# Kernel tuning notes

Measured on AMD Instinct MI355X. Metric: run time of the kernel, lower is better.

Reference implementation:

```python
import math
import jax, jax.numpy as jnp
import numpy as np

B, S, E = 4, 2048, 768
H, D = 12, 64
LOCAL_H, GLOBAL_H = 8, 4
WINDOW_BASE, MIN_W, MAX_W = 128, 32, 512
GLOBAL_RATIO = 0.1
MASK_VALUE = -1e9


def setup_inputs() -> dict:
    key = jax.random.key(0)
    k1, k2, k3 = jax.random.split(key, 3)
    return {
        "x": jax.random.normal(k1, (B, S, E), dtype=jnp.float32),
        "w_attn": jax.random.normal(k2, (E, 3 * E), dtype=jnp.float32) * 0.02,
        "b_attn": jnp.zeros((3 * E,), dtype=jnp.float32),
        "w_proj": jax.random.normal(k3, (E, E), dtype=jnp.float32) * 0.02,
        "b_proj": jnp.zeros((E,), dtype=jnp.float32),
    }


def _masks(seq_len: int):
    # dynamic window (adaptive): base * sqrt(S/base), clamped
    w = int(WINDOW_BASE * math.sqrt(seq_len / WINDOW_BASE))
    w = max(MIN_W, min(w, MAX_W))
    half = w // 2
    i = jnp.arange(seq_len)[:, None]
    j = jnp.arange(seq_len)[None, :]
    # local: window band then causal override -> allowed iff i-half <= j <= i
    local_allowed = (j >= i - half) & (j <= i)
    local_mask = jnp.where(local_allowed, 0.0, MASK_VALUE).astype(jnp.float32)
    # global: columns at linspace positions allowed for all rows, plus full causal
    n_glob = max(1, int(seq_len * GLOBAL_RATIO))
    gpos = jnp.linspace(0.0, seq_len - 1, n_glob).astype(jnp.int32)
    is_gcol = jnp.zeros((seq_len,), dtype=bool).at[gpos].set(True)
    global_allowed = (j <= i) | is_gcol[None, :]
    global_mask = jnp.where(global_allowed, 0.0, MASK_VALUE).astype(jnp.float32)
    return local_mask, global_mask


def _attend(q, k, v, mask):
    # q,k,v: [B,h,S,D]; mask: [S,S]
    scale = 1.0 / math.sqrt(q.shape[-1])
    scores = jnp.einsum("bhqd,bhkd->bhqk", q, k) * scale + mask[None, None]
    w = jax.nn.softmax(scores, axis=-1)
    return jnp.einsum("bhqk,bhkd->bhqd", w, v)


def reference(x, w_attn, b_attn, w_proj, b_proj):
    b, s, _ = x.shape
    qkv = x @ w_attn + b_attn                       # [B,S,3E]
    q, k, v = jnp.split(qkv, 3, axis=-1)
    def heads(t):
        return t.reshape(b, s, H, D).transpose(0, 2, 1, 3)  # [B,H,S,D]
    q, k, v = heads(q), heads(k), heads(v)
    local_mask, global_mask = _masks(s)
    local_out = _attend(q[:, :LOCAL_H], k[:, :LOCAL_H], v[:, :LOCAL_H], local_mask)
    global_out = _attend(q[:, LOCAL_H:], k[:, LOCAL_H:], v[:, LOCAL_H:], global_mask)
    attn = jnp.concatenate([local_out, global_out], axis=1)  # heads 0..7 local, 8..11 global
    attn = attn.transpose(0, 2, 1, 3).reshape(b, s, E)
    return attn @ w_proj + b_proj
```

## Files before the change

### kernel.cpp

```cpp
#include <hip/hip_runtime.h>
#include <stdint.h>


#define NH 12
#define SQ 2048

typedef __bf16 bf16x8 __attribute__((ext_vector_type(8)));
typedef float f32x4 __attribute__((ext_vector_type(4)));

#define GLOAD_LDS16(g, l)                                                      \
  __builtin_amdgcn_global_load_lds(                                            \
      (__attribute__((address_space(1))) void*)(g),                            \
      (__attribute__((address_space(3))) void*)(l), 16, 0, 0)

__device__ __forceinline__ unsigned short bfbits(float f) {
  __bf16 h = (__bf16)f;
  return *(unsigned short*)&h;
}

__global__ void convert_x(const float* __restrict__ in, unsigned short* __restrict__ outp, int n4) {
  for (int i = blockIdx.x * blockDim.x + threadIdx.x; i < n4; i += gridDim.x * blockDim.x) {
    float4 v = ((const float4*)in)[i];
    ushort4 o = make_ushort4(bfbits(v.x), bfbits(v.y), bfbits(v.z), bfbits(v.w));
    ((ushort4*)outp)[i] = o;
  }
}

__global__ void convert_transpose(const float* __restrict__ in, unsigned short* __restrict__ out,
                                  int K, int N) {
  __shared__ float tile[32][33];
  int n0 = blockIdx.x * 32, k0 = blockIdx.y * 32;
  int tx = threadIdx.x, ty = threadIdx.y;
  for (int r = ty; r < 32; r += 8) tile[r][tx] = in[(size_t)(k0 + r) * N + n0 + tx];
  __syncthreads();
  for (int r = ty; r < 32; r += 8) out[(size_t)(n0 + r) * K + k0 + tx] = bfbits(tile[tx][r]);
}

__global__ __launch_bounds__(256) void vtrans(const unsigned short* __restrict__ QKV,
                                              unsigned short* __restrict__ Vtb) {
  const int bh = blockIdx.x;
  const int b = bh / NH, h = bh % NH;
  const int s0 = blockIdx.y * 64;
  __shared__ unsigned short T[64][72];
  const int t = threadIdx.x, r = t >> 2, c0 = (t & 3) * 16;
  const size_t src = (size_t)(b * SQ + s0 + r) * 2304 + 1536 + h * 64 + c0;
  *(uint4*)&T[r][c0]     = *(const uint4*)&QKV[src];
  *(uint4*)&T[r][c0 + 8] = *(const uint4*)&QKV[src + 8];
  __syncthreads();
  unsigned short pk[16];
#pragma unroll
  for (int z = 0; z < 16; ++z) pk[z] = T[c0 + z][r];
  size_t dst = (size_t)bh * 131072 + (size_t)r * 2048 + s0 + c0;
  *(uint4*)&Vtb[dst]     = *(uint4*)&pk[0];
  *(uint4*)&Vtb[dst + 8] = *(uint4*)&pk[8];
}

__global__ void gather_gcols(const unsigned short* __restrict__ QKV,
                             const unsigned short* __restrict__ Vtb,
                             unsigned short* __restrict__ Kg,
                             unsigned short* __restrict__ VgT,
                             int* __restrict__ gidx) {
  const int bh = blockIdx.x;
  const int b = bh >> 2, h = 8 + (bh & 3);
  const int tid = threadIdx.x;
  if (bh == 0 && blockIdx.y == 0) {
    int c = tid;
    gidx[c] = (c < 203) ? (int)((double)c * (2047.0 / 203.0)) : ((c == 203) ? 2047 : -1);
  }
  {
    int c = tid, ch = blockIdx.y;
    int col = (c < 203) ? (int)((double)c * (2047.0 / 203.0)) : ((c == 203) ? 2047 : -1);
    uint4 v = {0u, 0u, 0u, 0u};
    if (col >= 0) v = *(const uint4*)&QKV[(size_t)(b * SQ + col) * 2304 + 768 + h * 64 + ch * 8];
    *(uint4*)&Kg[((size_t)bh * 256 + c) * 64 + ch * 8] = v;
  }
  {
    const size_t base = (size_t)(b * NH + h) * 131072;
    int d = tid >> 2;
    int cb = (tid & 3) * 64 + blockIdx.y * 8;
    for (int cc = 0; cc < 8; ++cc) {
      int c = cb + cc;
      int col = (c < 203) ? (int)((double)c * (2047.0 / 203.0)) : ((c == 203) ? 2047 : -1);
      unsigned short v = 0;
      if (col >= 0) v = Vtb[base + (size_t)d * 2048 + col];
      VgT[((size_t)bh * 64 + d) * 256 + c] = v;
    }
  }
}

__device__ __forceinline__ void gemm_mainloop(
    const unsigned short* __restrict__ A, const unsigned short* __restrict__ BT,
    int m0, int n0, int tid,
    unsigned short* As, unsigned short* Bs,
    f32x4 acc[4][4]) {
  const int lane = tid & 63, wave = tid >> 6;
  const int wm = wave >> 1, wn = wave & 1;
  const int ln = lane & 15, quad = lane >> 4;
  const int arow = wave * 16 + (lane >> 2);
  const int acol = (lane & 3) * 8;

#pragma unroll
  for (int mi = 0; mi < 4; ++mi)
#pragma unroll
    for (int ni = 0; ni < 4; ++ni) acc[mi][ni] = (f32x4){0.f, 0.f, 0.f, 0.f};

  for (int kt = 0; kt < 24; ++kt) {
    const int k0 = kt * 32;
    __syncthreads();
#pragma unroll
    for (int p = 0; p < 2; ++p) {
      GLOAD_LDS16(A  + (size_t)(m0 + p * 64 + arow) * 768 + k0 + acol,
                  &As[(p * 64 + wave * 16) * 32]);
      GLOAD_LDS16(BT + (size_t)(n0 + p * 64 + arow) * 768 + k0 + acol,
                  &Bs[(p * 64 + wave * 16) * 32]);
    }
    __syncthreads();
    bf16x8 aF[4], bF[4];
#pragma unroll
    for (int mi = 0; mi < 4; ++mi) aF[mi] = *(const bf16x8*)&As[(wm * 64 + mi * 16 + ln) * 32 + quad * 8];
#pragma unroll
    for (int ni = 0; ni < 4; ++ni) bF[ni] = *(const bf16x8*)&Bs[(wn * 64 + ni * 16 + ln) * 32 + quad * 8];
#pragma unroll
    for (int mi = 0; mi < 4; ++mi)
#pragma unroll
      for (int ni = 0; ni < 4; ++ni)
        acc[mi][ni] = __builtin_amdgcn_mfma_f32_16x16x32_bf16(aF[mi], bF[ni], acc[mi][ni], 0, 0, 0);
  }
}

__global__ __launch_bounds__(256) void qkv_gemm(
    const unsigned short* __restrict__ Xb, const unsigned short* __restrict__ WT,
    const float* __restrict__ bias, unsigned short* __restrict__ Out) {
  __shared__ __attribute__((aligned(16))) unsigned short As[128 * 32];
  __shared__ __attribute__((aligned(16))) unsigned short Bs[128 * 32];
  f32x4 acc[4][4];
  const int m0 = blockIdx.y * 128, n0 = blockIdx.x * 128;
  const int tid = threadIdx.x;
  gemm_mainloop(Xb, WT, m0, n0, tid, As, Bs, acc);
  const int lane = tid & 63, wave = tid >> 6;
  const int wm = wave >> 1, wn = wave & 1, ln = lane & 15, quad = lane >> 4;
#pragma unroll
  for (int mi = 0; mi < 4; ++mi)
#pragma unroll
    for (int ni = 0; ni < 4; ++ni) {
      int n = n0 + wn * 64 + ni * 16 + ln;
      float bs = bias[n];
#pragma unroll
      for (int rg = 0; rg < 4; ++rg) {
        int m = m0 + wm * 64 + mi * 16 + quad * 4 + rg;
        Out[(size_t)m * 2304 + n] = bfbits(acc[mi][ni][rg] + bs);
      }
    }
}

__global__ __launch_bounds__(256) void proj_gemm(
    const unsigned short* __restrict__ Ab, const unsigned short* __restrict__ WT,
    const float* __restrict__ bias, float* __restrict__ Out) {
  __shared__ __attribute__((aligned(16))) unsigned short As[128 * 32];
  __shared__ __attribute__((aligned(16))) unsigned short Bs[128 * 32];
  f32x4 acc[4][4];
  const int m0 = blockIdx.y * 128, n0 = blockIdx.x * 128;
  const int tid = threadIdx.x;
  gemm_mainloop(Ab, WT, m0, n0, tid, As, Bs, acc);
  const int lane = tid & 63, wave = tid >> 6;
  const int wm = wave >> 1, wn = wave & 1, ln = lane & 15, quad = lane >> 4;
#pragma unroll
  for (int mi = 0; mi < 4; ++mi)
#pragma unroll
    for (int ni = 0; ni < 4; ++ni)
#pragma unroll
      for (int rg = 0; rg < 4; ++rg) {
        int m = m0 + wm * 64 + mi * 16 + quad * 4 + rg;
        int n = n0 + wn * 64 + ni * 16 + ln;
        Out[(size_t)m * 768 + n] = acc[mi][ni][rg] + bias[n];
      }
}

__global__ __launch_bounds__(256, 6) void attn_kernel(
    const unsigned short* __restrict__ QKV,
    const unsigned short* __restrict__ Vtb,
    const unsigned short* __restrict__ Kg, const unsigned short* __restrict__ VgT,
    const int* __restrict__ gidx,
    unsigned short* __restrict__ AOut,
    unsigned short* __restrict__ Opart,
    float* __restrict__ Lpart) {
  __shared__ __attribute__((aligned(16))) unsigned short Ks[64 * 72];
  __shared__ __attribute__((aligned(16))) unsigned short Vs[64 * 72];

  const int gid = blockIdx.x;
  int b, h, qb, kb_begin, kb_end, slot = -1;
  bool do_g;
  if (gid < 1184) {
    int bh = gid / 74, rem = gid % 74;
    b = bh >> 2; h = 8 + (bh & 3);
    int part;
    if (rem < 9)       { qb = rem; part = 0; }
    else if (rem < 27) { int z = rem - 9;  qb = 9 + (z >> 1);  part = z & 1; }
    else if (rem < 54) { int z = rem - 27; int q3 = z / 3; qb = 18 + q3; part = z - 3 * q3; }
    else               { int z = rem - 54; qb = 27 + (z >> 2); part = z & 3; }
    kb_begin = part * 9;
    kb_end = min(part * 9 + 8, qb);
    do_g = (part == 0);
    slot = (bh * 32 + qb) * 4 + part;
  } else {
    int lid = gid - 1184;
    int bh = lid >> 5; b = bh >> 3; h = bh & 7; qb = lid & 31;
    kb_begin = (qb > 4) ? qb - 4 : 0; kb_end = qb; do_g = false;
  }
  const int qb0 = qb * 64;
  const bool is_local = (h < 8);
  const int tid = threadIdx.x, lane = tid & 63, wave = tid >> 6;
  const int ln = lane & 15, quad = lane >> 4;
  const int bh48 = b * NH + h;
  const int bhg = (b << 2) | (h & 3);

  const size_t qoff = (size_t)(b * SQ + qb0 + wave * 16 + ln) * 2304 + h * 64;
  bf16x8 qA0 = *(const bf16x8*)&QKV[qoff + quad * 8];
  bf16x8 qA1 = *(const bf16x8*)&QKV[qoff + 32 + quad * 8];

  bf16x8 onesF;
#pragma unroll
  for (int z = 0; z < 8; ++z) onesF[z] = (__bf16)1.0f;

  f32x4 o[4];
  f32x4 ls = (f32x4){0.f, 0.f, 0.f, 0.f};
#pragma unroll
  for (int dt = 0; dt < 4; ++dt) o[dt] = (f32x4){0.f, 0.f, 0.f, 0.f};

  const int nc = kb_end - kb_begin + 1;
  const int ntiles = nc + (do_g ? 4 : 0);
  const int irow = qb0 + wave * 16 + quad * 4;
  const int iw = qb0 + wave * 16;
  const int sr = tid >> 3, sch = tid & 7;

  for (int t = 0; t < ntiles; ++t) {
    const bool gph = (t >= nc);
    const int kstart = gph ? 0 : (kb_begin + t) * 64;
    const int kg0 = gph ? (t - nc) * 64 : 0;
    __syncthreads();
    if (!gph) {
#pragma unroll
      for (int p = 0; p < 2; ++p) {
        int row = p * 32 + sr;
        *(uint4*)&Ks[row * 72 + sch * 8] =
            *(const uint4*)&QKV[(size_t)(b * SQ + kstart + row) * 2304 + 768 + h * 64 + sch * 8];
        *(uint4*)&Vs[row * 72 + sch * 8] =
            *(const uint4*)&Vtb[(size_t)bh48 * 131072 + (size_t)row * 2048 + kstart + sch * 8];
      }
    } else {
#pragma unroll
      for (int p = 0; p < 2; ++p) {
        int row = p * 32 + sr;
        *(uint4*)&Ks[row * 72 + sch * 8] =
            *(const uint4*)&Kg[((size_t)bhg * 256 + kg0 + row) * 64 + sch * 8];
        *(uint4*)&Vs[row * 72 + sch * 8] =
            *(const uint4*)&VgT[((size_t)bhg * 64 + row) * 256 + kg0 + sch * 8];
      }
    }
    __syncthreads();

    float sc[4][4];
    const bool full = !gph && (kstart + 63 <= iw) && (!is_local || kstart >= iw - 241);
#pragma unroll
    for (int nt = 0; nt < 4; ++nt) {
      bf16x8 kF0 = *(const bf16x8*)&Ks[(nt * 16 + ln) * 72 + quad * 8];
      bf16x8 kF1 = *(const bf16x8*)&Ks[(nt * 16 + ln) * 72 + 32 + quad * 8];
      f32x4 c = (f32x4){0.f, 0.f, 0.f, 0.f};
      c = __builtin_amdgcn_mfma_f32_16x16x32_bf16(qA0, kF0, c, 0, 0, 0);
      c = __builtin_amdgcn_mfma_f32_16x16x32_bf16(qA1, kF1, c, 0, 0, 0);
      if (full) {
#pragma unroll
        for (int rg = 0; rg < 4; ++rg) sc[nt][rg] = c[rg] * 0.125f - 8.f;
      } else if (!gph) {
        int j = kstart + nt * 16 + ln;
#pragma unroll
        for (int rg = 0; rg < 4; ++rg) {
          int i = irow + rg;
          bool ok = is_local ? (j >= i - 256 && j <= i) : (j <= i);
          sc[nt][rg] = ok ? (c[rg] * 0.125f - 8.f) : -1e9f;
        }
      } else {
        int jg = gidx[kg0 + nt * 16 + ln];
#pragma unroll
        for (int rg = 0; rg < 4; ++rg) {
          bool ok = jg > (irow + rg);
          sc[nt][rg] = ok ? (c[rg] * 0.125f - 8.f) : -1e9f;
        }
      }
    }
    __syncthreads();

    __bf16* P = (__bf16*)Ks;
#pragma unroll
    for (int rg = 0; rg < 4; ++rg) {
      int prow = (wave * 16 + quad * 4 + rg) * 72;
#pragma unroll
      for (int nt = 0; nt < 4; ++nt)
        P[prow + nt * 16 + ln] = (__bf16)__expf(sc[nt][rg]);
    }
    bf16x8 pF0 = *(const bf16x8*)&Ks[(wave * 16 + ln) * 72 + quad * 8];
    bf16x8 pF1 = *(const bf16x8*)&Ks[(wave * 16 + ln) * 72 + 32 + quad * 8];
    ls = __builtin_amdgcn_mfma_f32_16x16x32_bf16(pF0, onesF, ls, 0, 0, 0);
    ls = __builtin_amdgcn_mfma_f32_16x16x32_bf16(pF1, onesF, ls, 0, 0, 0);
#pragma unroll
    for (int dt = 0; dt < 4; ++dt) {
      bf16x8 vF0 = *(const bf16x8*)&Vs[(dt * 16 + ln) * 72 + quad * 8];
      bf16x8 vF1 = *(const bf16x8*)&Vs[(dt * 16 + ln) * 72 + 32 + quad * 8];
      o[dt] = __builtin_amdgcn_mfma_f32_16x16x32_bf16(pF0, vF0, o[dt], 0, 0, 0);
      o[dt] = __builtin_amdgcn_mfma_f32_16x16x32_bf16(pF1, vF1, o[dt], 0, 0, 0);
    }
  }

  if (gid >= 1184) {
#pragma unroll
    for (int dt = 0; dt < 4; ++dt)
#pragma unroll
      for (int rg = 0; rg < 4; ++rg) {
        int row = b * SQ + qb0 + wave * 16 + quad * 4 + rg;
        int e = h * 64 + dt * 16 + ln;
        AOut[(size_t)row * 768 + e] = bfbits(o[dt][rg] / ls[rg]);
      }
  } else {
#pragma unroll
    for (int dt = 0; dt < 4; ++dt)
#pragma unroll
      for (int rg = 0; rg < 4; ++rg) {
        int row = wave * 16 + quad * 4 + rg;
        Opart[(size_t)slot * 4096 + row * 64 + dt * 16 + ln] = bfbits(o[dt][rg]);
      }
    if (ln == 0) {
#pragma unroll
      for (int rg = 0; rg < 4; ++rg)
        Lpart[(size_t)slot * 64 + wave * 16 + quad * 4 + rg] = ls[rg];
    }
  }
}

__global__ __launch_bounds__(256) void combine_parts(
    const unsigned short* __restrict__ Opart, const float* __restrict__ Lpart,
    unsigned short* __restrict__ AOut) {
  const int bid = blockIdx.x;
  const int bh = bid >> 5, qb = bid & 31;
  const int b = bh >> 2, h = 8 + (bh & 3);
  const int np = qb / 9 + 1;
  const int t = threadIdx.x, r = t >> 2, c0 = (t & 3) * 16;
  const int slot0 = (bh * 32 + qb) * 4;
  float acc[16];
#pragma unroll
  for (int z = 0; z < 16; ++z) acc[z] = 0.f;
  float l = 0.f;
  for (int p = 0; p < np; ++p) {
    const unsigned short* src = &Opart[(size_t)(slot0 + p) * 4096 + r * 64 + c0];
    bf16x8 v0 = *(const bf16x8*)&src[0];
    bf16x8 v1 = *(const bf16x8*)&src[8];
#pragma unroll
    for (int z = 0; z < 8; ++z) { acc[z] += (float)v0[z]; acc[8 + z] += (float)v1[z]; }
    l += Lpart[(size_t)(slot0 + p) * 64 + r];
  }
  float inv = 1.f / l;
  unsigned short pk[16];
#pragma unroll
  for (int z = 0; z < 16; ++z) pk[z] = bfbits(acc[z] * inv);
  size_t dst = (size_t)(b * SQ + qb * 64 + r) * 768 + h * 64 + c0;
  *(uint4*)&AOut[dst]     = *(uint4*)&pk[0];
  *(uint4*)&AOut[dst + 8] = *(uint4*)&pk[8];
}

extern "C" void kernel_launch(void* const* d_in, const int* in_sizes, int n_in,
                              void* d_out, int out_size, void* d_ws, size_t ws_size,
                              hipStream_t stream) {
  const float* x      = (const float*)d_in[0];
  const float* w_attn = (const float*)d_in[1];
  const float* b_attn = (const float*)d_in[2];
  const float* w_proj = (const float*)d_in[3];
  const float* b_proj = (const float*)d_in[4];
  float* out = (float*)d_out;

  char* ws = (char*)d_ws;
  size_t off = 0;
  auto alloc = [&](size_t bytes) {
    void* p = ws + off;
    off += (bytes + 255) & ~(size_t)255;
    return p;
  };
  unsigned short* xb     = (unsigned short*)alloc((size_t)8192 * 768 * 2);
  unsigned short* wattnT = (unsigned short*)alloc((size_t)2304 * 768 * 2);
  unsigned short* wprojT = (unsigned short*)alloc((size_t)768 * 768 * 2);
  unsigned short* qkvb   = (unsigned short*)alloc((size_t)8192 * 2304 * 2);
  unsigned short* Vtb    = (unsigned short*)alloc((size_t)48 * 64 * 2048 * 2);
  unsigned short* Kgb    = (unsigned short*)alloc((size_t)16 * 256 * 64 * 2);
  unsigned short* VgTb   = (unsigned short*)alloc((size_t)16 * 64 * 256 * 2);
  int* gidxb             = (int*)alloc((size_t)256 * 4);
  unsigned short* Opartb = (unsigned short*)alloc((size_t)2048 * 4096 * 2);
  float* Lpartb          = (float*)alloc((size_t)2048 * 64 * 4);
  unsigned short* attnb  = xb;

  convert_x<<<dim3(512), dim3(256), 0, stream>>>(x, xb, 8192 * 768 / 4);
  convert_transpose<<<dim3(72, 24), dim3(32, 8), 0, stream>>>(w_attn, wattnT, 768, 2304);
  convert_transpose<<<dim3(24, 24), dim3(32, 8), 0, stream>>>(w_proj, wprojT, 768, 768);

  qkv_gemm<<<dim3(18, 64), dim3(256), 0, stream>>>(xb, wattnT, b_attn, qkvb);
  vtrans<<<dim3(48, 32), dim3(256), 0, stream>>>(qkvb, Vtb);
  gather_gcols<<<dim3(16, 8), dim3(256), 0, stream>>>(qkvb, Vtb, Kgb, VgTb, gidxb);
  attn_kernel<<<dim3(2208), dim3(256), 0, stream>>>(qkvb, Vtb, Kgb, VgTb, gidxb,
                                                    attnb, Opartb, Lpartb);
  combine_parts<<<dim3(512), dim3(256), 0, stream>>>(Opartb, Lpartb, attnb);
  proj_gemm<<<dim3(6, 64), dim3(256), 0, stream>>>(attnb, wprojT, b_proj, out);
}
```

Before: 228.4 us.

## Double attention query tile to 128 rows, merge prep and gather kernels

```diff
diff --git a/kernel.cpp b/kernel.cpp
--- a/kernel.cpp
+++ b/kernel.cpp
@@ -18,71 +18,76 @@
   return *(unsigned short*)&h;
 }
 
-__global__ void convert_x(const float* __restrict__ in, unsigned short* __restrict__ outp, int n4) {
-  for (int i = blockIdx.x * blockDim.x + threadIdx.x; i < n4; i += gridDim.x * blockDim.x) {
-    float4 v = ((const float4*)in)[i];
-    ushort4 o = make_ushort4(bfbits(v.x), bfbits(v.y), bfbits(v.z), bfbits(v.w));
-    ((ushort4*)outp)[i] = o;
-  }
-}
-
-__global__ void convert_transpose(const float* __restrict__ in, unsigned short* __restrict__ out,
-                                  int K, int N) {
+__global__ __launch_bounds__(256) void prep(
+    const float* __restrict__ x, unsigned short* __restrict__ xb,
+    const float* __restrict__ w_attn, unsigned short* __restrict__ wattnT,
+    const float* __restrict__ w_proj, unsigned short* __restrict__ wprojT) {
+  const int bid = blockIdx.x, t = threadIdx.x;
+  if (bid < 512) {
+    const int n4 = 8192 * 768 / 4;
+    for (int i = bid * 256 + t; i < n4; i += 512 * 256) {
+      float4 v = ((const float4*)x)[i];
+      ((ushort4*)xb)[i] = make_ushort4(bfbits(v.x), bfbits(v.y), bfbits(v.z), bfbits(v.w));
+    }
+    return;
+  }
   __shared__ float tile[32][33];
-  int n0 = blockIdx.x * 32, k0 = blockIdx.y * 32;
-  int tx = threadIdx.x, ty = threadIdx.y;
+  const float* in; unsigned short* out; int K, N, tl;
+  if (bid < 512 + 72 * 24) { in = w_attn; out = wattnT; K = 768; N = 2304; tl = bid - 512; }
+  else                     { in = w_proj; out = wprojT; K = 768; N = 768;  tl = bid - 512 - 72 * 24; }
+  const int tpr = N / 32;
+  const int n0 = (tl % tpr) * 32, k0 = (tl / tpr) * 32;
+  const int tx = t & 31, ty = t >> 5;
   for (int r = ty; r < 32; r += 8) tile[r][tx] = in[(size_t)(k0 + r) * N + n0 + tx];
   __syncthreads();
   for (int r = ty; r < 32; r += 8) out[(size_t)(n0 + r) * K + k0 + tx] = bfbits(tile[tx][r]);
 }
 
-__global__ __launch_bounds__(256) void vtrans(const unsigned short* __restrict__ QKV,
-                                              unsigned short* __restrict__ Vtb) {
-  const int bh = blockIdx.x;
-  const int b = bh / NH, h = bh % NH;
-  const int s0 = blockIdx.y * 64;
-  __shared__ unsigned short T[64][72];
-  const int t = threadIdx.x, r = t >> 2, c0 = (t & 3) * 16;
-  const size_t src = (size_t)(b * SQ + s0 + r) * 2304 + 1536 + h * 64 + c0;
-  *(uint4*)&T[r][c0]     = *(const uint4*)&QKV[src];
-  *(uint4*)&T[r][c0 + 8] = *(const uint4*)&QKV[src + 8];
-  __syncthreads();
-  unsigned short pk[16];
-#pragma unroll
-  for (int z = 0; z < 16; ++z) pk[z] = T[c0 + z][r];
-  size_t dst = (size_t)bh * 131072 + (size_t)r * 2048 + s0 + c0;
-  *(uint4*)&Vtb[dst]     = *(uint4*)&pk[0];
-  *(uint4*)&Vtb[dst + 8] = *(uint4*)&pk[8];
-}
-
-__global__ void gather_gcols(const unsigned short* __restrict__ QKV,
-                             const unsigned short* __restrict__ Vtb,
-                             unsigned short* __restrict__ Kg,
-                             unsigned short* __restrict__ VgT,
-                             int* __restrict__ gidx) {
-  const int bh = blockIdx.x;
+__global__ __launch_bounds__(256) void vprep(const unsigned short* __restrict__ QKV,
+                                             unsigned short* __restrict__ Vtb,
+                                             unsigned short* __restrict__ Kg,
+                                             unsigned short* __restrict__ VgT,
+                                             int* __restrict__ gidx) {
+  const int id = blockIdx.x, t = threadIdx.x;
+  if (id < 1536) {
+    const int bh = id >> 5, b = bh / NH, h = bh % NH;
+    const int s0 = (id & 31) * 64;
+    __shared__ unsigned short T[64][72];
+    const int r = t >> 2, c0 = (t & 3) * 16;
+    const size_t src = (size_t)(b * SQ + s0 + r) * 2304 + 1536 + h * 64 + c0;
+    *(uint4*)&T[r][c0]     = *(const uint4*)&QKV[src];
+    *(uint4*)&T[r][c0 + 8] = *(const uint4*)&QKV[src + 8];
+    __syncthreads();
+    unsigned short pk[16];
+#pragma unroll
+    for (int z = 0; z < 16; ++z) pk[z] = T[c0 + z][r];
+    size_t dst = (size_t)bh * 131072 + (size_t)r * 2048 + s0 + c0;
+    *(uint4*)&Vtb[dst]     = *(uint4*)&pk[0];
+    *(uint4*)&Vtb[dst + 8] = *(uint4*)&pk[8];
+    return;
+  }
+  const int g = id - 1536;
+  const int bh = g >> 3, y = g & 7;
   const int b = bh >> 2, h = 8 + (bh & 3);
-  const int tid = threadIdx.x;
-  if (bh == 0 && blockIdx.y == 0) {
-    int c = tid;
+  if (g == 0) {
+    int c = t;
     gidx[c] = (c < 203) ? (int)((double)c * (2047.0 / 203.0)) : ((c == 203) ? 2047 : -1);
   }
   {
-    int c = tid, ch = blockIdx.y;
+    int c = t, ch = y;
     int col = (c < 203) ? (int)((double)c * (2047.0 / 203.0)) : ((c == 203) ? 2047 : -1);
     uint4 v = {0u, 0u, 0u, 0u};
     if (col >= 0) v = *(const uint4*)&QKV[(size_t)(b * SQ + col) * 2304 + 768 + h * 64 + ch * 8];
     *(uint4*)&Kg[((size_t)bh * 256 + c) * 64 + ch * 8] = v;
   }
   {
-    const size_t base = (size_t)(b * NH + h) * 131072;
-    int d = tid >> 2;
-    int cb = (tid & 3) * 64 + blockIdx.y * 8;
+    int d = t >> 2;
+    int cb = (t & 3) * 64 + y * 8;
     for (int cc = 0; cc < 8; ++cc) {
       int c = cb + cc;
       int col = (c < 203) ? (int)((double)c * (2047.0 / 203.0)) : ((c == 203) ? 2047 : -1);
       unsigned short v = 0;
-      if (col >= 0) v = Vtb[base + (size_t)d * 2048 + col];
+      if (col >= 0) v = QKV[(size_t)(b * SQ + col) * 2304 + 1536 + h * 64 + d];
       VgT[((size_t)bh * 64 + d) * 256 + c] = v;
     }
   }
@@ -176,7 +181,7 @@
       }
 }
 
-__global__ __launch_bounds__(256, 6) void attn_kernel(
+__global__ __launch_bounds__(256, 4) void attn_kernel(
     const unsigned short* __restrict__ QKV,
     const unsigned short* __restrict__ Vtb,
     const unsigned short* __restrict__ Kg, const unsigned short* __restrict__ VgT,
@@ -188,49 +193,56 @@
   __shared__ __attribute__((aligned(16))) unsigned short Vs[64 * 72];
 
   const int gid = blockIdx.x;
-  int b, h, qb, kb_begin, kb_end, slot = -1;
-  bool do_g;
-  if (gid < 1184) {
-    int bh = gid / 74, rem = gid % 74;
+  int b, h, qi, kb_begin, kb_end, slot = 0;
+  bool do_g = false, multi = false;
+  if (gid < 608) {
+    int bh = gid / 38, rem = gid % 38;
     b = bh >> 2; h = 8 + (bh & 3);
     int part;
-    if (rem < 9)       { qb = rem; part = 0; }
-    else if (rem < 27) { int z = rem - 9;  qb = 9 + (z >> 1);  part = z & 1; }
-    else if (rem < 54) { int z = rem - 27; int q3 = z / 3; qb = 18 + q3; part = z - 3 * q3; }
-    else               { int z = rem - 54; qb = 27 + (z >> 2); part = z & 3; }
-    kb_begin = part * 9;
-    kb_end = min(part * 9 + 8, qb);
+    if (rem < 4)       { qi = rem; part = 0; }
+    else if (rem < 14) { int z = rem - 4;  qi = 4 + (z >> 1); part = z & 1; }
+    else if (rem < 26) { int z = rem - 14; int q3 = z / 3; qi = 9 + q3; part = z - 3 * q3; }
+    else               { int z = rem - 26; qi = 13 + (z >> 2); part = z & 3; }
+    kb_begin = 9 * part;
+    kb_end = min(9 * part + 8, 2 * qi + 1);
     do_g = (part == 0);
-    slot = (bh * 32 + qb) * 4 + part;
+    multi = (qi >= 4);
+    slot = (bh * 16 + qi) * 4 + part;
   } else {
-    int lid = gid - 1184;
-    int bh = lid >> 5; b = bh >> 3; h = bh & 7; qb = lid & 31;
-    kb_begin = (qb > 4) ? qb - 4 : 0; kb_end = qb; do_g = false;
-  }
-  const int qb0 = qb * 64;
+    int lid = gid - 608;
+    int bh = lid >> 4; b = bh >> 3; h = bh & 7; qi = lid & 15;
+    kb_begin = max(0, 2 * qi - 4); kb_end = 2 * qi + 1;
+  }
+  const int qb0 = qi * 128;
   const bool is_local = (h < 8);
   const int tid = threadIdx.x, lane = tid & 63, wave = tid >> 6;
   const int ln = lane & 15, quad = lane >> 4;
   const int bh48 = b * NH + h;
   const int bhg = (b << 2) | (h & 3);
 
-  const size_t qoff = (size_t)(b * SQ + qb0 + wave * 16 + ln) * 2304 + h * 64;
-  bf16x8 qA0 = *(const bf16x8*)&QKV[qoff + quad * 8];
-  bf16x8 qA1 = *(const bf16x8*)&QKV[qoff + 32 + quad * 8];
+  bf16x8 qA[2][2];
+#pragma unroll
+  for (int s = 0; s < 2; ++s) {
+    const size_t qoff = (size_t)(b * SQ + qb0 + wave * 32 + s * 16 + ln) * 2304 + h * 64;
+    qA[s][0] = *(const bf16x8*)&QKV[qoff + quad * 8];
+    qA[s][1] = *(const bf16x8*)&QKV[qoff + 32 + quad * 8];
+  }
 
   bf16x8 onesF;
 #pragma unroll
   for (int z = 0; z < 8; ++z) onesF[z] = (__bf16)1.0f;
 
-  f32x4 o[4];
-  f32x4 ls = (f32x4){0.f, 0.f, 0.f, 0.f};
-#pragma unroll
-  for (int dt = 0; dt < 4; ++dt) o[dt] = (f32x4){0.f, 0.f, 0.f, 0.f};
+  f32x4 o[2][4], ls2[2];
+#pragma unroll
+  for (int s = 0; s < 2; ++s) {
+    ls2[s] = (f32x4){0.f, 0.f, 0.f, 0.f};
+#pragma unroll
+    for (int dt = 0; dt < 4; ++dt) o[s][dt] = (f32x4){0.f, 0.f, 0.f, 0.f};
+  }
 
   const int nc = kb_end - kb_begin + 1;
   const int ntiles = nc + (do_g ? 4 : 0);
-  const int irow = qb0 + wave * 16 + quad * 4;
-  const int iw = qb0 + wave * 16;
+  const int iw = qb0 + wave * 32;
   const int sr = tid >> 3, sch = tid & 7;
 
   for (int t = 0; t < ntiles; ++t) {
@@ -259,79 +271,90 @@
     }
     __syncthreads();
 
-    float sc[4][4];
-    const bool full = !gph && (kstart + 63 <= iw) && (!is_local || kstart >= iw - 241);
+    float p2[2][4][4];
+    const bool full = !gph && (kstart + 63 <= iw) && (!is_local || kstart >= iw - 225);
 #pragma unroll
     for (int nt = 0; nt < 4; ++nt) {
       bf16x8 kF0 = *(const bf16x8*)&Ks[(nt * 16 + ln) * 72 + quad * 8];
       bf16x8 kF1 = *(const bf16x8*)&Ks[(nt * 16 + ln) * 72 + 32 + quad * 8];
-      f32x4 c = (f32x4){0.f, 0.f, 0.f, 0.f};
-      c = __builtin_amdgcn_mfma_f32_16x16x32_bf16(qA0, kF0, c, 0, 0, 0);
-      c = __builtin_amdgcn_mfma_f32_16x16x32_bf16(qA1, kF1, c, 0, 0, 0);
-      if (full) {
-#pragma unroll
-        for (int rg = 0; rg < 4; ++rg) sc[nt][rg] = c[rg] * 0.125f - 8.f;
-      } else if (!gph) {
-        int j = kstart + nt * 16 + ln;
+#pragma unroll
+      for (int s = 0; s < 2; ++s) {
+        f32x4 c = (f32x4){0.f, 0.f, 0.f, 0.f};
+        c = __builtin_amdgcn_mfma_f32_16x16x32_bf16(qA[s][0], kF0, c, 0, 0, 0);
+        c = __builtin_amdgcn_mfma_f32_16x16x32_bf16(qA[s][1], kF1, c, 0, 0, 0);
+        if (full) {
+#pragma unroll
+          for (int rg = 0; rg < 4; ++rg) p2[s][nt][rg] = __expf(c[rg] * 0.125f - 8.f);
+        } else if (!gph) {
+          int j = kstart + nt * 16 + ln;
+#pragma unroll
+          for (int rg = 0; rg < 4; ++rg) {
+            int i = iw + s * 16 + quad * 4 + rg;
+            bool ok = is_local ? (j >= i - 256 && j <= i) : (j <= i);
+            p2[s][nt][rg] = ok ? __expf(c[rg] * 0.125f - 8.f) : 0.f;
+          }
+        } else {
+          int jg = gidx[kg0 + nt * 16 + ln];
+#pragma unroll
+          for (int rg = 0; rg < 4; ++rg) {
+            bool ok = jg > (iw + s * 16 + quad * 4 + rg);
+            p2[s][nt][rg] = ok ? __expf(c[rg] * 0.125f - 8.f) : 0.f;
+          }
+        }
+      }
+    }
+    __syncthreads();
+
+    __bf16* P = (__bf16*)Ks;
+#pragma unroll
+    for (int s = 0; s < 2; ++s) {
+#pragma unroll
+      for (int rg = 0; rg < 4; ++rg) {
+        int prow = (wave * 16 + quad * 4 + rg) * 72;
+#pragma unroll
+        for (int nt = 0; nt < 4; ++nt)
+          P[prow + nt * 16 + ln] = (__bf16)p2[s][nt][rg];
+      }
+      bf16x8 pF0 = *(const bf16x8*)&Ks[(wave * 16 + ln) * 72 + quad * 8];
+      bf16x8 pF1 = *(const bf16x8*)&Ks[(wave * 16 + ln) * 72 + 32 + quad * 8];
+      ls2[s] = __builtin_amdgcn_mfma_f32_16x16x32_bf16(pF0, onesF, ls2[s], 0, 0, 0);
+      ls2[s] = __builtin_amdgcn_mfma_f32_16x16x32_bf16(pF1, onesF, ls2[s], 0, 0, 0);
+#pragma unroll
+      for (int dt = 0; dt < 4; ++dt) {
+        bf16x8 vF0 = *(const bf16x8*)&Vs[(dt * 16 + ln) * 72 + quad * 8];
+        bf16x8 vF1 = *(const bf16x8*)&Vs[(dt * 16 + ln) * 72 + 32 + quad * 8];
+        o[s][dt] = __builtin_amdgcn_mfma_f32_16x16x32_bf16(pF0, vF0, o[s][dt], 0, 0, 0);
+        o[s][dt] = __builtin_amdgcn_mfma_f32_16x16x32_bf16(pF1, vF1, o[s][dt], 0, 0, 0);
+      }
+    }
+  }
+
+  if (gid >= 608 || !multi) {
+#pragma unroll
+    for (int s = 0; s < 2; ++s)
+#pragma unroll
+      for (int dt = 0; dt < 4; ++dt)
 #pragma unroll
         for (int rg = 0; rg < 4; ++rg) {
-          int i = irow + rg;
-          bool ok = is_local ? (j >= i - 256 && j <= i) : (j <= i);
-          sc[nt][rg] = ok ? (c[rg] * 0.125f - 8.f) : -1e9f;
+          int row = b * SQ + qb0 + wave * 32 + s * 16 + quad * 4 + rg;
+          int e = h * 64 + dt * 16 + ln;
+          AOut[(size_t)row * 768 + e] = bfbits(o[s][dt][rg] / ls2[s][rg]);
         }
-      } else {
-        int jg = gidx[kg0 + nt * 16 + ln];
+  } else {
+#pragma unroll
+    for (int s = 0; s < 2; ++s) {
+#pragma unroll
+      for (int dt = 0; dt < 4; ++dt)
 #pragma unroll
         for (int rg = 0; rg < 4; ++rg) {
-          bool ok = jg > (irow + rg);
-          sc[nt][rg] = ok ? (c[rg] * 0.125f - 8.f) : -1e9f;
+          int row = wave * 32 + s * 16 + quad * 4 + rg;
+          Opart[(size_t)slot * 8192 + row * 64 + dt * 16 + ln] = bfbits(o[s][dt][rg]);
         }
-      }
-    }
-    __syncthreads();
-
-    __bf16* P = (__bf16*)Ks;
-#pragma unroll
-    for (int rg = 0; rg < 4; ++rg) {
-      int prow = (wave * 16 + quad * 4 + rg) * 72;
-#pragma unroll
-      for (int nt = 0; nt < 4; ++nt)
-        P[prow + nt * 16 + ln] = (__bf16)__expf(sc[nt][rg]);
-    }
-    bf16x8 pF0 = *(const bf16x8*)&Ks[(wave * 16 + ln) * 72 + quad * 8];
-    bf16x8 pF1 = *(const bf16x8*)&Ks[(wave * 16 + ln) * 72 + 32 + quad * 8];
-    ls = __builtin_amdgcn_mfma_f32_16x16x32_bf16(pF0, onesF, ls, 0, 0, 0);
-    ls = __builtin_amdgcn_mfma_f32_16x16x32_bf16(pF1, onesF, ls, 0, 0, 0);
-#pragma unroll
-    for (int dt = 0; dt < 4; ++dt) {
-      bf16x8 vF0 = *(const bf16x8*)&Vs[(dt * 16 + ln) * 72 + quad * 8];
-      bf16x8 vF1 = *(const bf16x8*)&Vs[(dt * 16 + ln) * 72 + 32 + quad * 8];
-      o[dt] = __builtin_amdgcn_mfma_f32_16x16x32_bf16(pF0, vF0, o[dt], 0, 0, 0);
-      o[dt] = __builtin_amdgcn_mfma_f32_16x16x32_bf16(pF1, vF1, o[dt], 0, 0, 0);
-    }
-  }
-
-  if (gid >= 1184) {
-#pragma unroll
-    for (int dt = 0; dt < 4; ++dt)
-#pragma unroll
-      for (int rg = 0; rg < 4; ++rg) {
-        int row = b * SQ + qb0 + wave * 16 + quad * 4 + rg;
-        int e = h * 64 + dt * 16 + ln;
-        AOut[(size_t)row * 768 + e] = bfbits(o[dt][rg] / ls[rg]);
-      }
-  } else {
-#pragma unroll
-    for (int dt = 0; dt < 4; ++dt)
-#pragma unroll
-      for (int rg = 0; rg < 4; ++rg) {
-        int row = wave * 16 + quad * 4 + rg;
-        Opart[(size_t)slot * 4096 + row * 64 + dt * 16 + ln] = bfbits(o[dt][rg]);
-      }
-    if (ln == 0) {
-#pragma unroll
-      for (int rg = 0; rg < 4; ++rg)
-        Lpart[(size_t)slot * 64 + wave * 16 + quad * 4 + rg] = ls[rg];
+      if (ln == 0) {
+#pragma unroll
+        for (int rg = 0; rg < 4; ++rg)
+          Lpart[(size_t)slot * 128 + wave * 32 + s * 16 + quad * 4 + rg] = ls2[s][rg];
+      }
     }
   }
 }
@@ -340,30 +363,32 @@
     const unsigned short* __restrict__ Opart, const float* __restrict__ Lpart,
     unsigned short* __restrict__ AOut) {
   const int bid = blockIdx.x;
-  const int bh = bid >> 5, qb = bid & 31;
+  const int bh = bid / 12, qi = bid % 12 + 4;
   const int b = bh >> 2, h = 8 + (bh & 3);
-  const int np = qb / 9 + 1;
-  const int t = threadIdx.x, r = t >> 2, c0 = (t & 3) * 16;
-  const int slot0 = (bh * 32 + qb) * 4;
-  float acc[16];
-#pragma unroll
-  for (int z = 0; z < 16; ++z) acc[z] = 0.f;
+  const int np = (qi <= 8) ? 2 : ((qi <= 12) ? 3 : 4);
+  const int t = threadIdx.x, r = t >> 1, c0 = (t & 1) * 32;
+  const int slot0 = (bh * 16 + qi) * 4;
+  float acc[32];
+#pragma unroll
+  for (int z = 0; z < 32; ++z) acc[z] = 0.f;
   float l = 0.f;
   for (int p = 0; p < np; ++p) {
-    const unsigned short* src = &Opart[(size_t)(slot0 + p) * 4096 + r * 64 + c0];
-    bf16x8 v0 = *(const bf16x8*)&src[0];
-    bf16x8 v1 = *(const bf16x8*)&src[8];
-#pragma unroll
-    for (int z = 0; z < 8; ++z) { acc[z] += (float)v0[z]; acc[8 + z] += (float)v1[z]; }
-    l += Lpart[(size_t)(slot0 + p) * 64 + r];
+    const unsigned short* src = &Opart[(size_t)(slot0 + p) * 8192 + r * 64 + c0];
+#pragma unroll
+    for (int q = 0; q < 4; ++q) {
+      bf16x8 v = *(const bf16x8*)&src[q * 8];
+#pragma unroll
+      for (int z = 0; z < 8; ++z) acc[q * 8 + z] += (float)v[z];
+    }
+    l += Lpart[(size_t)(slot0 + p) * 128 + r];
   }
   float inv = 1.f / l;
-  unsigned short pk[16];
-#pragma unroll
-  for (int z = 0; z < 16; ++z) pk[z] = bfbits(acc[z] * inv);
-  size_t dst = (size_t)(b * SQ + qb * 64 + r) * 768 + h * 64 + c0;
-  *(uint4*)&AOut[dst]     = *(uint4*)&pk[0];
-  *(uint4*)&AOut[dst + 8] = *(uint4*)&pk[8];
+  unsigned short pk[32];
+#pragma unroll
+  for (int z = 0; z < 32; ++z) pk[z] = bfbits(acc[z] * inv);
+  size_t dst = (size_t)(b * SQ + qi * 128 + r) * 768 + h * 64 + c0;
+#pragma unroll
+  for (int q = 0; q < 4; ++q) *(uint4*)&AOut[dst + q * 8] = *(uint4*)&pk[q * 8];
 }
 
 extern "C" void kernel_launch(void* const* d_in, const int* in_sizes, int n_in,
@@ -391,19 +416,16 @@
   unsigned short* Kgb    = (unsigned short*)alloc((size_t)16 * 256 * 64 * 2);
   unsigned short* VgTb   = (unsigned short*)alloc((size_t)16 * 64 * 256 * 2);
   int* gidxb             = (int*)alloc((size_t)256 * 4);
-  unsigned short* Opartb = (unsigned short*)alloc((size_t)2048 * 4096 * 2);
-  float* Lpartb          = (float*)alloc((size_t)2048 * 64 * 4);
+  unsigned short* Opartb = (unsigned short*)alloc((size_t)1024 * 8192 * 2);
+  float* Lpartb          = (float*)alloc((size_t)1024 * 128 * 4);
   unsigned short* attnb  = xb;
 
-  convert_x<<<dim3(512), dim3(256), 0, stream>>>(x, xb, 8192 * 768 / 4);
-  convert_transpose<<<dim3(72, 24), dim3(32, 8), 0, stream>>>(w_attn, wattnT, 768, 2304);
-  convert_transpose<<<dim3(24, 24), dim3(32, 8), 0, stream>>>(w_proj, wprojT, 768, 768);
-
+  prep<<<dim3(512 + 72 * 24 + 24 * 24), dim3(256), 0, stream>>>(
+      x, xb, w_attn, wattnT, w_proj, wprojT);
   qkv_gemm<<<dim3(18, 64), dim3(256), 0, stream>>>(xb, wattnT, b_attn, qkvb);
-  vtrans<<<dim3(48, 32), dim3(256), 0, stream>>>(qkvb, Vtb);
-  gather_gcols<<<dim3(16, 8), dim3(256), 0, stream>>>(qkvb, Vtb, Kgb, VgTb, gidxb);
-  attn_kernel<<<dim3(2208), dim3(256), 0, stream>>>(qkvb, Vtb, Kgb, VgTb, gidxb,
+  vprep<<<dim3(1536 + 128), dim3(256), 0, stream>>>(qkvb, Vtb, Kgb, VgTb, gidxb);
+  attn_kernel<<<dim3(1120), dim3(256), 0, stream>>>(qkvb, Vtb, Kgb, VgTb, gidxb,
                                                     attnb, Opartb, Lpartb);
-  combine_parts<<<dim3(512), dim3(256), 0, stream>>>(Opartb, Lpartb, attnb);
+  combine_parts<<<dim3(192), dim3(256), 0, stream>>>(Opartb, Lpartb, attnb);
   proj_gemm<<<dim3(6, 64), dim3(256), 0, stream>>>(attnb, wprojT, b_proj, out);
 }
```

Measured after the change: 240.3 us. 5.2% more time.

## Merge prep kernels and register-prefetch next K/V tile in attention loop

Applied to the files above, without the earlier changes.

```diff
diff --git a/kernel.cpp b/kernel.cpp
--- a/kernel.cpp
+++ b/kernel.cpp
@@ -18,71 +18,76 @@
   return *(unsigned short*)&h;
 }
 
-__global__ void convert_x(const float* __restrict__ in, unsigned short* __restrict__ outp, int n4) {
-  for (int i = blockIdx.x * blockDim.x + threadIdx.x; i < n4; i += gridDim.x * blockDim.x) {
-    float4 v = ((const float4*)in)[i];
-    ushort4 o = make_ushort4(bfbits(v.x), bfbits(v.y), bfbits(v.z), bfbits(v.w));
-    ((ushort4*)outp)[i] = o;
-  }
-}
-
-__global__ void convert_transpose(const float* __restrict__ in, unsigned short* __restrict__ out,
-                                  int K, int N) {
+__global__ __launch_bounds__(256) void prep(
+    const float* __restrict__ x, unsigned short* __restrict__ xb,
+    const float* __restrict__ w_attn, unsigned short* __restrict__ wattnT,
+    const float* __restrict__ w_proj, unsigned short* __restrict__ wprojT) {
+  const int bid = blockIdx.x, t = threadIdx.x;
+  if (bid < 512) {
+    const int n4 = 8192 * 768 / 4;
+    for (int i = bid * 256 + t; i < n4; i += 512 * 256) {
+      float4 v = ((const float4*)x)[i];
+      ((ushort4*)xb)[i] = make_ushort4(bfbits(v.x), bfbits(v.y), bfbits(v.z), bfbits(v.w));
+    }
+    return;
+  }
   __shared__ float tile[32][33];
-  int n0 = blockIdx.x * 32, k0 = blockIdx.y * 32;
-  int tx = threadIdx.x, ty = threadIdx.y;
+  const float* in; unsigned short* out; int K, N, tl;
+  if (bid < 512 + 72 * 24) { in = w_attn; out = wattnT; K = 768; N = 2304; tl = bid - 512; }
+  else                     { in = w_proj; out = wprojT; K = 768; N = 768;  tl = bid - 512 - 72 * 24; }
+  const int tpr = N / 32;
+  const int n0 = (tl % tpr) * 32, k0 = (tl / tpr) * 32;
+  const int tx = t & 31, ty = t >> 5;
   for (int r = ty; r < 32; r += 8) tile[r][tx] = in[(size_t)(k0 + r) * N + n0 + tx];
   __syncthreads();
   for (int r = ty; r < 32; r += 8) out[(size_t)(n0 + r) * K + k0 + tx] = bfbits(tile[tx][r]);
 }
 
-__global__ __launch_bounds__(256) void vtrans(const unsigned short* __restrict__ QKV,
-                                              unsigned short* __restrict__ Vtb) {
-  const int bh = blockIdx.x;
-  const int b = bh / NH, h = bh % NH;
-  const int s0 = blockIdx.y * 64;
-  __shared__ unsigned short T[64][72];
-  const int t = threadIdx.x, r = t >> 2, c0 = (t & 3) * 16;
-  const size_t src = (size_t)(b * SQ + s0 + r) * 2304 + 1536 + h * 64 + c0;
-  *(uint4*)&T[r][c0]     = *(const uint4*)&QKV[src];
-  *(uint4*)&T[r][c0 + 8] = *(const uint4*)&QKV[src + 8];
-  __syncthreads();
-  unsigned short pk[16];
-#pragma unroll
-  for (int z = 0; z < 16; ++z) pk[z] = T[c0 + z][r];
-  size_t dst = (size_t)bh * 131072 + (size_t)r * 2048 + s0 + c0;
-  *(uint4*)&Vtb[dst]     = *(uint4*)&pk[0];
-  *(uint4*)&Vtb[dst + 8] = *(uint4*)&pk[8];
-}
-
-__global__ void gather_gcols(const unsigned short* __restrict__ QKV,
-                             const unsigned short* __restrict__ Vtb,
-                             unsigned short* __restrict__ Kg,
-                             unsigned short* __restrict__ VgT,
-                             int* __restrict__ gidx) {
-  const int bh = blockIdx.x;
+__global__ __launch_bounds__(256) void vprep(const unsigned short* __restrict__ QKV,
+                                             unsigned short* __restrict__ Vtb,
+                                             unsigned short* __restrict__ Kg,
+                                             unsigned short* __restrict__ VgT,
+                                             int* __restrict__ gidx) {
+  const int id = blockIdx.x, t = threadIdx.x;
+  if (id < 1536) {
+    const int bh = id >> 5, b = bh / NH, h = bh % NH;
+    const int s0 = (id & 31) * 64;
+    __shared__ unsigned short T[64][72];
+    const int r = t >> 2, c0 = (t & 3) * 16;
+    const size_t src = (size_t)(b * SQ + s0 + r) * 2304 + 1536 + h * 64 + c0;
+    *(uint4*)&T[r][c0]     = *(const uint4*)&QKV[src];
+    *(uint4*)&T[r][c0 + 8] = *(const uint4*)&QKV[src + 8];
+    __syncthreads();
+    unsigned short pk[16];
+#pragma unroll
+    for (int z = 0; z < 16; ++z) pk[z] = T[c0 + z][r];
+    size_t dst = (size_t)bh * 131072 + (size_t)r * 2048 + s0 + c0;
+    *(uint4*)&Vtb[dst]     = *(uint4*)&pk[0];
+    *(uint4*)&Vtb[dst + 8] = *(uint4*)&pk[8];
+    return;
+  }
+  const int g = id - 1536;
+  const int bh = g >> 3, y = g & 7;
   const int b = bh >> 2, h = 8 + (bh & 3);
-  const int tid = threadIdx.x;
-  if (bh == 0 && blockIdx.y == 0) {
-    int c = tid;
+  if (g == 0) {
+    int c = t;
     gidx[c] = (c < 203) ? (int)((double)c * (2047.0 / 203.0)) : ((c == 203) ? 2047 : -1);
   }
   {
-    int c = tid, ch = blockIdx.y;
+    int c = t, ch = y;
     int col = (c < 203) ? (int)((double)c * (2047.0 / 203.0)) : ((c == 203) ? 2047 : -1);
     uint4 v = {0u, 0u, 0u, 0u};
     if (col >= 0) v = *(const uint4*)&QKV[(size_t)(b * SQ + col) * 2304 + 768 + h * 64 + ch * 8];
     *(uint4*)&Kg[((size_t)bh * 256 + c) * 64 + ch * 8] = v;
   }
   {
-    const size_t base = (size_t)(b * NH + h) * 131072;
-    int d = tid >> 2;
-    int cb = (tid & 3) * 64 + blockIdx.y * 8;
+    int d = t >> 2;
+    int cb = (t & 3) * 64 + y * 8;
     for (int cc = 0; cc < 8; ++cc) {
       int c = cb + cc;
       int col = (c < 203) ? (int)((double)c * (2047.0 / 203.0)) : ((c == 203) ? 2047 : -1);
       unsigned short v = 0;
-      if (col >= 0) v = Vtb[base + (size_t)d * 2048 + col];
+      if (col >= 0) v = QKV[(size_t)(b * SQ + col) * 2304 + 1536 + h * 64 + d];
       VgT[((size_t)bh * 64 + d) * 256 + c] = v;
     }
   }
@@ -188,8 +193,8 @@
   __shared__ __attribute__((aligned(16))) unsigned short Vs[64 * 72];
 
   const int gid = blockIdx.x;
-  int b, h, qb, kb_begin, kb_end, slot = -1;
-  bool do_g;
+  int b, h, qb, kb_begin, kb_end, slot = 0;
+  bool do_g = false;
   if (gid < 1184) {
     int bh = gid / 74, rem = gid % 74;
     b = bh >> 2; h = 8 + (bh & 3);
@@ -201,11 +206,11 @@
     kb_begin = part * 9;
     kb_end = min(part * 9 + 8, qb);
     do_g = (part == 0);
-    slot = (bh * 32 + qb) * 4 + part;
+    slot = ((b * 4 + (h - 8)) * 32 + qb) * 4 + part;
   } else {
     int lid = gid - 1184;
     int bh = lid >> 5; b = bh >> 3; h = bh & 7; qb = lid & 31;
-    kb_begin = (qb > 4) ? qb - 4 : 0; kb_end = qb; do_g = false;
+    kb_begin = (qb > 4) ? qb - 4 : 0; kb_end = qb;
   }
   const int qb0 = qb * 64;
   const bool is_local = (h < 8);
@@ -233,31 +238,42 @@
   const int iw = qb0 + wave * 16;
   const int sr = tid >> 3, sch = tid & 7;
 
+  uint4 kpre[2], vpre[2];
+  auto prefetch = [&](int t) {
+    const bool gph = (t >= nc);
+    if (!gph) {
+      const int kstart = (kb_begin + t) * 64;
+#pragma unroll
+      for (int p = 0; p < 2; ++p) {
+        int row = p * 32 + sr;
+        kpre[p] = *(const uint4*)&QKV[(size_t)(b * SQ + kstart + row) * 2304 + 768 + h * 64 + sch * 8];
+        vpre[p] = *(const uint4*)&Vtb[(size_t)bh48 * 131072 + (size_t)row * 2048 + kstart + sch * 8];
+      }
+    } else {
+      const int kg0 = (t - nc) * 64;
+#pragma unroll
+      for (int p = 0; p < 2; ++p) {
+        int row = p * 32 + sr;
+        kpre[p] = *(const uint4*)&Kg[((size_t)bhg * 256 + kg0 + row) * 64 + sch * 8];
+        vpre[p] = *(const uint4*)&VgT[((size_t)bhg * 64 + row) * 256 + kg0 + sch * 8];
+      }
+    }
+  };
+  prefetch(0);
+
   for (int t = 0; t < ntiles; ++t) {
     const bool gph = (t >= nc);
     const int kstart = gph ? 0 : (kb_begin + t) * 64;
     const int kg0 = gph ? (t - nc) * 64 : 0;
     __syncthreads();
-    if (!gph) {
-#pragma unroll
-      for (int p = 0; p < 2; ++p) {
-        int row = p * 32 + sr;
-        *(uint4*)&Ks[row * 72 + sch * 8] =
-            *(const uint4*)&QKV[(size_t)(b * SQ + kstart + row) * 2304 + 768 + h * 64 + sch * 8];
-        *(uint4*)&Vs[row * 72 + sch * 8] =
-            *(const uint4*)&Vtb[(size_t)bh48 * 131072 + (size_t)row * 2048 + kstart + sch * 8];
-      }
-    } else {
-#pragma unroll
-      for (int p = 0; p < 2; ++p) {
-        int row = p * 32 + sr;
-        *(uint4*)&Ks[row * 72 + sch * 8] =
-            *(const uint4*)&Kg[((size_t)bhg * 256 + kg0 + row) * 64 + sch * 8];
-        *(uint4*)&Vs[row * 72 + sch * 8] =
-            *(const uint4*)&VgT[((size_t)bhg * 64 + row) * 256 + kg0 + sch * 8];
-      }
-    }
-    __syncthreads();
+#pragma unroll
+    for (int p = 0; p < 2; ++p) {
+      int row = p * 32 + sr;
+      *(uint4*)&Ks[row * 72 + sch * 8] = kpre[p];
+      *(uint4*)&Vs[row * 72 + sch * 8] = vpre[p];
+    }
+    __syncthreads();
+    if (t + 1 < ntiles) prefetch(t + 1);
 
     float sc[4][4];
     const bool full = !gph && (kstart + 63 <= iw) && (!is_local || kstart >= iw - 241);
@@ -395,13 +411,10 @@
   float* Lpartb          = (float*)alloc((size_t)2048 * 64 * 4);
   unsigned short* attnb  = xb;
 
-  convert_x<<<dim3(512), dim3(256), 0, stream>>>(x, xb, 8192 * 768 / 4);
-  convert_transpose<<<dim3(72, 24), dim3(32, 8), 0, stream>>>(w_attn, wattnT, 768, 2304);
-  convert_transpose<<<dim3(24, 24), dim3(32, 8), 0, stream>>>(w_proj, wprojT, 768, 768);
-
+  prep<<<dim3(512 + 72 * 24 + 24 * 24), dim3(256), 0, stream>>>(
+      x, xb, w_attn, wattnT, w_proj, wprojT);
   qkv_gemm<<<dim3(18, 64), dim3(256), 0, stream>>>(xb, wattnT, b_attn, qkvb);
-  vtrans<<<dim3(48, 32), dim3(256), 0, stream>>>(qkvb, Vtb);
-  gather_gcols<<<dim3(16, 8), dim3(256), 0, stream>>>(qkvb, Vtb, Kgb, VgTb, gidxb);
+  vprep<<<dim3(1536 + 128), dim3(256), 0, stream>>>(qkvb, Vtb, Kgb, VgTb, gidxb);
   attn_kernel<<<dim3(2208), dim3(256), 0, stream>>>(qkvb, Vtb, Kgb, VgTb, gidxb,
                                                     attnb, Opartb, Lpartb);
   combine_parts<<<dim3(512), dim3(256), 0, stream>>>(Opartb, Lpartb, attnb);
```

New measurement: 274.8 us. +20.4%, slower.
